# Performance work log

Measured on AMD Instinct MI355X. Metric: run time of the kernel, lower is better.

The kernel has to match this reference:

```python
import jax, jax.numpy as jnp
import numpy as np

ALPHA = 0.1        # ista() default lambda (module-level alpha is unused in this path)
N_ITERS = 50       # fixed iteration count replacing tolerance-based early exit
POWER_ITERS = 20   # power iterations to estimate Lipschitz constant L = ||Wd||_2^2


def _soft_threshold(x, t):
    return jnp.sign(x) * jnp.maximum(jnp.abs(x) - t, 0.0)


def _lipschitz(Wd):
    # largest eigenvalue of Wd^T Wd via power iteration
    v = jnp.ones((Wd.shape[1],), Wd.dtype)
    def body(v, _):
        v = Wd.T @ (Wd @ v)
        v = v / (jnp.linalg.norm(v) + 1e-12)
        return v, None
    v, _ = jax.lax.scan(body, v, None, length=POWER_ITERS)
    return jnp.vdot(v, Wd.T @ (Wd @ v)) / (jnp.vdot(v, v) + 1e-12)


def _ista(X, Wd):
    # X: [B, D], Wd: [D, K] -> sparse codes Z: [B, K]
    L = jax.lax.stop_gradient(_lipschitz(Wd))
    step = 1.0 / L
    Z0 = jnp.zeros((X.shape[0], Wd.shape[1]), X.dtype)
    def body(Z, _):
        grad = (Z @ Wd.T - X) @ Wd          # [B,D] @ [D,K] -> [B,K]
        Z = _soft_threshold(Z - step * grad, step * ALPHA)
        return Z, None
    Z, _ = jax.lax.scan(body, Z0, None, length=N_ITERS)
    return Z


def setup_inputs() -> dict:
    key = jax.random.key(0)
    k1, k2 = jax.random.split(key)
    z_e_x = jax.random.normal(k1, (8192, 16, 8, 8), jnp.float32)   # [B,C,H,W]
    dictionary = jax.random.normal(k2, (1024, 512), jnp.float32)   # [D,K], D=H*W*C
    return {"z_e_x": z_e_x, "dictionary": dictionary}


def reference(z_e_x, dictionary):
    B = z_e_x.shape[0]
    # permute(0,2,3,1).flatten(start_dim=1): [B,C,H,W] -> [B, H*W*C]
    X = jnp.transpose(z_e_x, (0, 2, 3, 1)).reshape(B, -1)
    Z = _ista(X, dictionary)                                  # [B,K]
    sparsity = jnp.sum(jnp.abs(Z) > 1e-6) / B
    outputs = (dictionary @ Z.T).T                            # [B,D]
    # torch code views back to z_e_x.shape WITHOUT inverse permute; replicate exactly
    return outputs.reshape(z_e_x.shape), sparsity
```

## Files before the change

kernel.cpp:

```cpp
#include <hip/hip_runtime.h>
#include <math.h>

#define BATCH 8192
#define DIM 1024
#define KDIM 512
#define ALPHA_C 0.1f
#define N_ITERS 50
#define ROWS 32
#define ZSH 512
#define HC 3
#define SEG 256

typedef short bf16x8 __attribute__((ext_vector_type(8)));
typedef float f32x4 __attribute__((ext_vector_type(4)));

__device__ __forceinline__ short f2bf(float x) {
  union { float f; unsigned u; } v; v.f = x;
  unsigned r = v.u + 0x7fffu + ((v.u >> 16) & 1u);
  return (short)(r >> 16);
}
__device__ __forceinline__ float bf2f(short s) {
  union { float f; unsigned u; } v;
  v.u = ((unsigned)(unsigned short)s) << 16;
  return v.f;
}

__device__ __forceinline__ int zswz(int row, int col) {
  return row * ZSH + ((((col >> 3) ^ (row & 15)) << 3) | (col & 7));
}
__device__ __forceinline__ int zoff8(int row, int colg) {
  return row * ZSH + ((colg ^ (row & 15)) << 3);
}

__global__ __launch_bounds__(256) void k_mmT_part(const float* __restrict__ A,
                                                  const float* __restrict__ B,
                                                  float* __restrict__ P) {
  int tx = (threadIdx.x & 15) * 2;
  int ty = (threadIdx.x >> 4) * 2;
  int a0 = blockIdx.y * 32 + ty;
  int b0 = blockIdx.x * 32 + tx;
  int j0 = blockIdx.z * SEG;
  float a00 = 0.f, a01 = 0.f, a10 = 0.f, a11 = 0.f;
  for (int j = j0; j < j0 + SEG; j += 8) {
#pragma unroll
    for (int u = 0; u < 8; ++u) {
      float2 av = *(const float2*)&A[(size_t)(j + u) * KDIM + a0];
      float2 bv = *(const float2*)&B[(size_t)(j + u) * KDIM + b0];
      a00 += av.x * bv.x;
      a01 += av.x * bv.y;
      a10 += av.y * bv.x;
      a11 += av.y * bv.y;
    }
  }
  float* P0 = P + (size_t)blockIdx.z * KDIM * KDIM;
  *(float2*)&P0[(size_t)a0 * KDIM + b0] = make_float2(a00, a01);
  *(float2*)&P0[(size_t)(a0 + 1) * KDIM + b0] = make_float2(a10, a11);
}

__global__ __launch_bounds__(256) void k_red(const float* __restrict__ P,
                                             float* __restrict__ C, int S,
                                             float scale) {
  int t = blockIdx.x * 256 + threadIdx.x;
  f32x4 s = (f32x4){0.f, 0.f, 0.f, 0.f};
  for (int z = 0; z < S; ++z) {
    f32x4 p = *(const f32x4*)&P[(size_t)z * KDIM * KDIM + t * 4];
    s.x += p.x; s.y += p.y; s.z += p.z; s.w += p.w;
  }
  s.x *= scale; s.y *= scale; s.z *= scale; s.w *= scale;
  *(f32x4*)&C[t * 4] = s;
}

__global__ __launch_bounds__(1024) void k_power_fast(
    const float* __restrict__ G4, const float* __restrict__ G8,
    const float* __restrict__ G, float* __restrict__ scal) {
  __shared__ float v[KDIM];
  __shared__ float part[1024];
  __shared__ double red[16];
  __shared__ double red2[16];
  __shared__ float stot;
  int tid = threadIdx.x;
  int lane = tid & 63, wid = tid >> 6;
  int col = tid & 511, h = tid >> 9;
  if (h == 0) v[col] = 1.0f;
  __syncthreads();

  const float* mats[3] = {G4, G8, G8};
#pragma unroll
  for (int s = 0; s < 3; ++s) {
    const float* gp = mats[s] + (size_t)(h * 256) * KDIM + col;
    const float* vp = v + h * 256;
    float a0 = 0.f, a1 = 0.f, a2 = 0.f, a3 = 0.f;
#pragma unroll 4
    for (int j = 0; j < 256; j += 4) {
      a0 += gp[(size_t)(j + 0) * KDIM] * vp[j + 0];
      a1 += gp[(size_t)(j + 1) * KDIM] * vp[j + 1];
      a2 += gp[(size_t)(j + 2) * KDIM] * vp[j + 2];
      a3 += gp[(size_t)(j + 3) * KDIM] * vp[j + 3];
    }
    part[tid] = (a0 + a1) + (a2 + a3);
    __syncthreads();
    float u = 0.f;
    double ssq = 0.0;
    if (h == 0) {
      u = part[col] + part[col + 512];
      ssq = (double)u * (double)u;
    }
#pragma unroll
    for (int off = 32; off; off >>= 1) ssq += __shfl_xor(ssq, off);
    if (lane == 0) red[wid] = ssq;
    __syncthreads();
    if (tid == 0) {
      double t = 0.0;
      for (int i = 0; i < 16; ++i) t += red[i];
      stot = (float)(sqrt(t) + 1e-12);
    }
    __syncthreads();
    if (h == 0) v[col] = u / stot;
    __syncthreads();
  }

  {
    const float* gp = G + (size_t)(h * 256) * KDIM + col;
    const float* vp = v + h * 256;
    float a0 = 0.f, a1 = 0.f, a2 = 0.f, a3 = 0.f;
#pragma unroll 4
    for (int j = 0; j < 256; j += 4) {
      a0 += gp[(size_t)(j + 0) * KDIM] * vp[j + 0];
      a1 += gp[(size_t)(j + 1) * KDIM] * vp[j + 1];
      a2 += gp[(size_t)(j + 2) * KDIM] * vp[j + 2];
      a3 += gp[(size_t)(j + 3) * KDIM] * vp[j + 3];
    }
    part[tid] = (a0 + a1) + (a2 + a3);
    __syncthreads();
    double nu = 0.0, de = 0.0;
    if (h == 0) {
      float u = part[col] + part[col + 512];
      nu = (double)v[col] * (double)u;
      de = (double)v[col] * (double)v[col];
    }
#pragma unroll
    for (int off = 32; off; off >>= 1) {
      nu += __shfl_xor(nu, off);
      de += __shfl_xor(de, off);
    }
    if (lane == 0) { red[wid] = nu; red2[wid] = de; }
    __syncthreads();
    if (tid == 0) {
      double n = 0.0, d = 0.0;
      for (int i = 0; i < 16; ++i) { n += red[i]; d += red2[i]; }
      float L = (float)(n / (d + 1e-12));
      float step = 1.0f / L;
      scal[0] = step;
      scal[1] = step * ALPHA_C;
    }
  }
}

__global__ __launch_bounds__(256) void k_pack_h(const float* __restrict__ G,
                                                const float* __restrict__ scal,
                                                short* __restrict__ Hh) {
  int t = blockIdx.x * 256 + threadIdx.x;
  int k = t >> 9, n = t & 511;
  float step = scal[0];
  float h = ((k == n) ? 1.0f : 0.0f) - step * G[k * KDIM + n];
  int kk = k >> 5, q = (k >> 3) & 3, j = k & 7;
  Hh[((size_t)((kk * 4 + q) * 512 + n)) * 8 + j] = f2bf(h);
}

__global__ __launch_bounds__(256) void k_pack_w(const float* __restrict__ Wd,
                                                const float* __restrict__ scal,
                                                short* __restrict__ Wh) {
  int t = blockIdx.x * 256 + threadIdx.x;
  int k = t >> 9, n = t & 511;
  float w = scal[0] * Wd[k * KDIM + n];
  int kk = k >> 5, q = (k >> 3) & 3, j = k & 7;
  Wh[((size_t)((kk * 4 + q) * 512 + n)) * 8 + j] = f2bf(w);
}

__global__ __launch_bounds__(256) void k_pack_wt(const float* __restrict__ Wd,
                                                 short* __restrict__ Wh) {
  int t = blockIdx.x * 256 + threadIdx.x;
  int k = t >> 10, n = t & 1023;
  float w = Wd[n * KDIM + k];
  int kk = k >> 5, q = (k >> 3) & 3, j = k & 7;
  Wh[((size_t)((kk * 4 + q) * 1024 + n)) * 8 + j] = f2bf(w);
}

__global__ __launch_bounds__(1024) void k_ista(
    const float* __restrict__ zex, const short* __restrict__ Hh,
    const short* __restrict__ Wph, const short* __restrict__ Wth,
    const float* __restrict__ scal, float* __restrict__ out,
    int* __restrict__ gcnt) {
  __shared__ short Zb[2][ROWS * ZSH];
  __shared__ short Hl2[HC * 16384];
  int tid = threadIdx.x;
  int lane = tid & 63, wid = tid >> 6;
  int l15 = lane & 15, lq = lane >> 4;
  int rb = blockIdx.x * ROWS;
  float thr = scal[1];

  f32x4 cs[2][2];
#pragma unroll
  for (int rf = 0; rf < 2; ++rf)
#pragma unroll
    for (int cf = 0; cf < 2; ++cf) cs[rf][cf] = (f32x4){0.f, 0.f, 0.f, 0.f};

  int sr = tid >> 5;
  int sc = (tid & 31) >> 1;
  int ph = tid & 1;
  for (int half = 0; half < 2; ++half) {
    __syncthreads();
    {
      const float* src =
          &zex[(size_t)(rb + sr) * DIM + sc * 64 + half * 32 + ph * 16];
#pragma unroll
      for (int m = 0; m < 16; m += 4) {
        float4 xv = *(const float4*)&src[m];
        float xs[4] = {xv.x, xv.y, xv.z, xv.w};
#pragma unroll
        for (int e = 0; e < 4; ++e) {
          int mm = ph * 16 + m + e;
          int dd = ((mm >> 3) << 7) + ((mm & 7) << 4) + sc;
          Zb[0][zswz(sr, dd)] = f2bf(xs[e]);
        }
      }
    }
    __syncthreads();
#pragma unroll 2
    for (int kk = 0; kk < 16; ++kk) {
      int kkg = half * 16 + kk;
      bf16x8 a[2];
#pragma unroll
      for (int rf = 0; rf < 2; ++rf)
        a[rf] = *(const bf16x8*)&Zb[0][zoff8(rf * 16 + l15, kk * 4 + lq)];
#pragma unroll
      for (int cf = 0; cf < 2; ++cf) {
        int n = wid * 32 + cf * 16 + l15;
        bf16x8 bh = *(const bf16x8*)&Wph[((size_t)((kkg * 4 + lq) * 512 + n)) * 8];
#pragma unroll
        for (int rf = 0; rf < 2; ++rf)
          cs[rf][cf] = __builtin_amdgcn_mfma_f32_16x16x32_bf16(a[rf], bh, cs[rf][cf], 0, 0, 0);
      }
    }
  }
  __syncthreads();

  for (int i = tid * 8; i < HC * 16384; i += 8192)
    *(bf16x8*)&Hl2[i] = *(const bf16x8*)&Hh[i];

#pragma unroll
  for (int rf = 0; rf < 2; ++rf)
#pragma unroll
    for (int cf = 0; cf < 2; ++cf) {
      int col = wid * 32 + cf * 16 + l15;
#pragma unroll
      for (int e = 0; e < 4; ++e) {
        float pre = cs[rf][cf][e];
        float mag = fmaxf(fabsf(pre) - thr, 0.f);
        float z = (pre >= 0.f) ? mag : -mag;
        int row = rf * 16 + lq * 4 + e;
        Zb[0][zswz(row, col)] = f2bf(z);
      }
    }
  __syncthreads();

  int cur = 0;
#pragma unroll 1
  for (int it = 1; it < N_ITERS; ++it) {
    int rot = it & 15;
    f32x4 acc[2][2];

    {
      int kkr = rot;
      bf16x8 a[2];
#pragma unroll
      for (int rf = 0; rf < 2; ++rf)
        a[rf] = *(const bf16x8*)&Zb[cur][zoff8(rf * 16 + l15, kkr * 4 + lq)];
#pragma unroll
      for (int cf = 0; cf < 2; ++cf) {
        int n = wid * 32 + cf * 16 + l15;
        size_t off = ((size_t)((kkr * 4 + lq) * 512 + n)) * 8;
        bf16x8 bh = (kkr < HC) ? *(const bf16x8*)&Hl2[off]
                               : *(const bf16x8*)&Hh[off];
#pragma unroll
        for (int rf = 0; rf < 2; ++rf)
          acc[rf][cf] = __builtin_amdgcn_mfma_f32_16x16x32_bf16(a[rf], bh, cs[rf][cf], 0, 0, 0);
      }
    }
#pragma unroll 2
    for (int kk = 1; kk < 16; ++kk) {
      int kkr = (kk + rot) & 15;
      bf16x8 a[2];
#pragma unroll
      for (int rf = 0; rf < 2; ++rf)
        a[rf] = *(const bf16x8*)&Zb[cur][zoff8(rf * 16 + l15, kkr * 4 + lq)];
#pragma unroll
      for (int cf = 0; cf < 2; ++cf) {
        int n = wid * 32 + cf * 16 + l15;
        size_t off = ((size_t)((kkr * 4 + lq) * 512 + n)) * 8;
        bf16x8 bh = (kkr < HC) ? *(const bf16x8*)&Hl2[off]
                               : *(const bf16x8*)&Hh[off];
#pragma unroll
        for (int rf = 0; rf < 2; ++rf)
          acc[rf][cf] = __builtin_amdgcn_mfma_f32_16x16x32_bf16(a[rf], bh, acc[rf][cf], 0, 0, 0);
      }
    }
#pragma unroll
    for (int rf = 0; rf < 2; ++rf)
#pragma unroll
      for (int cf = 0; cf < 2; ++cf) {
        int col = wid * 32 + cf * 16 + l15;
#pragma unroll
        for (int e = 0; e < 4; ++e) {
          float pre = acc[rf][cf][e];
          float mag = fmaxf(fabsf(pre) - thr, 0.f);
          float z = (pre >= 0.f) ? mag : -mag;
          int row = rf * 16 + lq * 4 + e;
          Zb[cur ^ 1][zswz(row, col)] = f2bf(z);
        }
      }
    cur ^= 1;
    __syncthreads();
  }

  int cnt = 0;
#pragma unroll 4
  for (int i = tid; i < ROWS * ZSH; i += 1024)
    cnt += (fabsf(bf2f(Zb[cur][i])) > 1e-6f) ? 1 : 0;
#pragma unroll
  for (int off = 32; off; off >>= 1) cnt += __shfl_xor(cnt, off);
  if (lane == 0) atomicAdd(gcnt, cnt);

  {
    f32x4 o[2][4];
#pragma unroll
    for (int rf = 0; rf < 2; ++rf)
#pragma unroll
      for (int cf = 0; cf < 4; ++cf) o[rf][cf] = (f32x4){0.f, 0.f, 0.f, 0.f};

#pragma unroll 2
    for (int kk = 0; kk < 16; ++kk) {
      bf16x8 a[2];
#pragma unroll
      for (int rf = 0; rf < 2; ++rf)
        a[rf] = *(const bf16x8*)&Zb[cur][zoff8(rf * 16 + l15, kk * 4 + lq)];
#pragma unroll
      for (int cf = 0; cf < 4; ++cf) {
        int n = wid * 64 + cf * 16 + l15;
        bf16x8 bh = *(const bf16x8*)&Wth[((size_t)((kk * 4 + lq) * 1024 + n)) * 8];
#pragma unroll
        for (int rf = 0; rf < 2; ++rf)
          o[rf][cf] = __builtin_amdgcn_mfma_f32_16x16x32_bf16(a[rf], bh, o[rf][cf], 0, 0, 0);
      }
    }
#pragma unroll
    for (int rf = 0; rf < 2; ++rf)
#pragma unroll
      for (int cf = 0; cf < 4; ++cf) {
        int col = wid * 64 + cf * 16 + l15;
#pragma unroll
        for (int e = 0; e < 4; ++e) {
          int row = rb + rf * 16 + lq * 4 + e;
          out[(size_t)row * DIM + col] = o[rf][cf][e];
        }
      }
  }
}

__global__ void k_final(const int* __restrict__ gcnt, float* __restrict__ out) {
  out[(size_t)BATCH * DIM] = (float)(*gcnt) / (float)BATCH;
}

extern "C" void kernel_launch(void* const* d_in, const int* in_sizes, int n_in,
                              void* d_out, int out_size, void* d_ws,
                              size_t ws_size, hipStream_t stream) {
  (void)in_sizes; (void)n_in; (void)out_size; (void)ws_size;
  const float* zex = (const float*)d_in[0];
  const float* Wd = (const float*)d_in[1];
  float* out = (float*)d_out;
  char* ws = (char*)d_ws;

  float* G = (float*)ws;
  float* G2 = (float*)(ws + (1 << 20));
  float* G4 = (float*)(ws + 2 * (1 << 20));
  float* G8 = (float*)(ws + 3 * (1 << 20));
  short* Hh = (short*)(ws + 4 * (1 << 20));
  short* Wph = (short*)(ws + 4 * (1 << 20) + (512 << 10));
  short* Wth = (short*)(ws + 5 * (1 << 20) + (512 << 10));
  float* scal = (float*)(ws + 6 * (1 << 20) + (512 << 10));
  int* gcnt = (int*)(ws + 6 * (1 << 20) + (512 << 10) + 64);
  float* PG = (float*)(ws + 1 * (1 << 20));
  float* PG2 = (float*)(ws + 2 * (1 << 20));
  float* PG4 = (float*)(ws + 3 * (1 << 20));
  float* PG8 = (float*)(ws + 4 * (1 << 20));

  hipMemsetAsync(gcnt, 0, sizeof(int), stream);
  k_mmT_part<<<dim3(16, 16, 4), 256, 0, stream>>>(Wd, Wd, PG);
  k_red<<<256, 256, 0, stream>>>(PG, G, 4, 1.0f);
  k_mmT_part<<<dim3(16, 16, 2), 256, 0, stream>>>(G, G, PG2);
  k_red<<<256, 256, 0, stream>>>(PG2, G2, 2, 9.5367431640625e-07f);
  k_mmT_part<<<dim3(16, 16, 2), 256, 0, stream>>>(G2, G2, PG4);
  k_red<<<256, 256, 0, stream>>>(PG4, G4, 2, 1.0f);
  k_mmT_part<<<dim3(16, 16, 2), 256, 0, stream>>>(G4, G4, PG8);
  k_red<<<256, 256, 0, stream>>>(PG8, G8, 2, 1.0f);
  k_power_fast<<<1, 1024, 0, stream>>>(G4, G8, G, scal);
  k_pack_h<<<1024, 256, 0, stream>>>(G, scal, Hh);
  k_pack_w<<<2048, 256, 0, stream>>>(Wd, scal, Wph);
  k_pack_wt<<<2048, 256, 0, stream>>>(Wd, Wth);
  k_ista<<<BATCH / ROWS, 1024, 0, stream>>>(zex, Hh, Wph, Wth, scal, out, gcnt);
  k_final<<<1, 1, 0, stream>>>(gcnt, out);
}
```

Baseline: 545.6 us.

## Run ISTA iterations with FP8 MFMA on scaled off-diagonal H and FP8 Z

Measured after the change: 536.3 us. No clear change (-1.7%).

```diff
diff --git a/kernel.cpp b/kernel.cpp
--- a/kernel.cpp
+++ b/kernel.cpp
@@ -8,11 +8,14 @@
 #define N_ITERS 50
 #define ROWS 32
 #define ZSH 512
-#define HC 3
 #define SEG 256
+#define SH 32.0f
+#define SZ 16.0f
+#define INVS 0.001953125f
 
 typedef short bf16x8 __attribute__((ext_vector_type(8)));
 typedef float f32x4 __attribute__((ext_vector_type(4)));
+typedef long longx2 __attribute__((ext_vector_type(2)));
 
 __device__ __forceinline__ short f2bf(float x) {
   union { float f; unsigned u; } v; v.f = x;
@@ -30,6 +33,10 @@
 }
 __device__ __forceinline__ int zoff8(int row, int colg) {
   return row * ZSH + ((colg ^ (row & 15)) << 3);
+}
+__device__ __forceinline__ int z8a(int row, int c) {
+  int g = ((((c >> 3) & 3) << 4) | (c >> 5)) ^ (row & 14);
+  return row * 512 + g * 8 + (c & 7);
 }
 
 __global__ __launch_bounds__(256) void k_mmT_part(const float* __restrict__ A,
@@ -156,15 +163,19 @@
   }
 }
 
-__global__ __launch_bounds__(256) void k_pack_h(const float* __restrict__ G,
-                                                const float* __restrict__ scal,
-                                                short* __restrict__ Hh) {
+__global__ __launch_bounds__(256) void k_pack_h8(const float* __restrict__ G,
+                                                 const float* __restrict__ scal,
+                                                 char* __restrict__ H8,
+                                                 float* __restrict__ hd) {
   int t = blockIdx.x * 256 + threadIdx.x;
   int k = t >> 9, n = t & 511;
   float step = scal[0];
-  float h = ((k == n) ? 1.0f : 0.0f) - step * G[k * KDIM + n];
-  int kk = k >> 5, q = (k >> 3) & 3, j = k & 7;
-  Hh[((size_t)((kk * 4 + q) * 512 + n)) * 8 + j] = f2bf(h);
+  float g = G[k * KDIM + n];
+  if (k == n) hd[n] = 1.0f - step * g;
+  float h = (k == n) ? 0.f : (-step * g) * SH;
+  int p = __builtin_amdgcn_cvt_pk_fp8_f32(h, h, 0, false);
+  size_t off = ((size_t)((k >> 5) * 4 + ((k >> 3) & 3))) * 4096 + n * 8 + (k & 7);
+  H8[off] = (char)(p & 0xff);
 }
 
 __global__ __launch_bounds__(256) void k_pack_w(const float* __restrict__ Wd,
@@ -187,12 +198,12 @@
 }
 
 __global__ __launch_bounds__(1024) void k_ista(
-    const float* __restrict__ zex, const short* __restrict__ Hh,
-    const short* __restrict__ Wph, const short* __restrict__ Wth,
-    const float* __restrict__ scal, float* __restrict__ out,
-    int* __restrict__ gcnt) {
-  __shared__ short Zb[2][ROWS * ZSH];
-  __shared__ short Hl2[HC * 16384];
+    const float* __restrict__ zex, const char* __restrict__ H8,
+    const float* __restrict__ hd, const short* __restrict__ Wph,
+    const short* __restrict__ Wth, const float* __restrict__ scal,
+    float* __restrict__ out, int* __restrict__ gcnt) {
+  __shared__ short Xb[ROWS * ZSH];
+  __shared__ char Z8[2][ROWS * 512];
   int tid = threadIdx.x;
   int lane = tid & 63, wid = tid >> 6;
   int l15 = lane & 15, lq = lane >> 4;
@@ -221,7 +232,7 @@
         for (int e = 0; e < 4; ++e) {
           int mm = ph * 16 + m + e;
           int dd = ((mm >> 3) << 7) + ((mm & 7) << 4) + sc;
-          Zb[0][zswz(sr, dd)] = f2bf(xs[e]);
+          Xb[zswz(sr, dd)] = f2bf(xs[e]);
         }
       }
     }
@@ -232,7 +243,7 @@
       bf16x8 a[2];
 #pragma unroll
       for (int rf = 0; rf < 2; ++rf)
-        a[rf] = *(const bf16x8*)&Zb[0][zoff8(rf * 16 + l15, kk * 4 + lq)];
+        a[rf] = *(const bf16x8*)&Xb[zoff8(rf * 16 + l15, kk * 4 + lq)];
 #pragma unroll
       for (int cf = 0; cf < 2; ++cf) {
         int n = wid * 32 + cf * 16 + l15;
@@ -245,9 +256,10 @@
   }
   __syncthreads();
 
-  for (int i = tid * 8; i < HC * 16384; i += 8192)
-    *(bf16x8*)&Hl2[i] = *(const bf16x8*)&Hh[i];
-
+  float hd0 = hd[wid * 32 + l15];
+  float hd1 = hd[wid * 32 + 16 + l15];
+
+  float zreg[2][2][4];
 #pragma unroll
   for (int rf = 0; rf < 2; ++rf)
 #pragma unroll
@@ -258,65 +270,68 @@
         float pre = cs[rf][cf][e];
         float mag = fmaxf(fabsf(pre) - thr, 0.f);
         float z = (pre >= 0.f) ? mag : -mag;
-        int row = rf * 16 + lq * 4 + e;
-        Zb[0][zswz(row, col)] = f2bf(z);
+        zreg[rf][cf][e] = z;
+        int pk = __builtin_amdgcn_cvt_pk_fp8_f32(z * SZ, z * SZ, 0, false);
+        Z8[0][z8a(rf * 16 + lq * 4 + e, col)] = (char)(pk & 0xff);
       }
     }
   __syncthreads();
+
+  int key = l15 & 14;
+  int abase0 = l15 * 512 + lq * 128;
+  int abase1 = (16 + l15) * 512 + lq * 128;
+  int vb = lq * 4096 + (wid * 32 + l15) * 8;
 
   int cur = 0;
 #pragma unroll 1
   for (int it = 1; it < N_ITERS; ++it) {
-    int rot = it & 15;
     f32x4 acc[2][2];
-
-    {
-      int kkr = rot;
-      bf16x8 a[2];
-#pragma unroll
-      for (int rf = 0; rf < 2; ++rf)
-        a[rf] = *(const bf16x8*)&Zb[cur][zoff8(rf * 16 + l15, kkr * 4 + lq)];
+#pragma unroll
+    for (int rf = 0; rf < 2; ++rf)
+#pragma unroll
+      for (int cf = 0; cf < 2; ++cf) acc[rf][cf] = (f32x4){0.f, 0.f, 0.f, 0.f};
+
+    int ks = (it & 7) << 1;
+#define ISTA_BODY(kk)                                                         \
+  {                                                                           \
+    int ao = ((kk) ^ key) * 8;                                                \
+    longx2 a0 = *(const longx2*)&Z8[cur][abase0 + ao];                        \
+    longx2 a1 = *(const longx2*)&Z8[cur][abase1 + ao];                        \
+    const char* hp = H8 + (size_t)(kk)*16384;                                 \
+    long b00 = *(const long*)&hp[vb];                                         \
+    long b01 = *(const long*)&hp[vb + 128];                                   \
+    long b10 = *(const long*)&hp[vb + 16384];                                 \
+    long b11 = *(const long*)&hp[vb + 16384 + 128];                           \
+    acc[0][0] = __builtin_amdgcn_mfma_f32_16x16x32_fp8_fp8(a0.x, b00, acc[0][0], 0, 0, 0); \
+    acc[1][0] = __builtin_amdgcn_mfma_f32_16x16x32_fp8_fp8(a1.x, b00, acc[1][0], 0, 0, 0); \
+    acc[0][1] = __builtin_amdgcn_mfma_f32_16x16x32_fp8_fp8(a0.x, b01, acc[0][1], 0, 0, 0); \
+    acc[1][1] = __builtin_amdgcn_mfma_f32_16x16x32_fp8_fp8(a1.x, b01, acc[1][1], 0, 0, 0); \
+    acc[0][0] = __builtin_amdgcn_mfma_f32_16x16x32_fp8_fp8(a0.y, b10, acc[0][0], 0, 0, 0); \
+    acc[1][0] = __builtin_amdgcn_mfma_f32_16x16x32_fp8_fp8(a1.y, b10, acc[1][0], 0, 0, 0); \
+    acc[0][1] = __builtin_amdgcn_mfma_f32_16x16x32_fp8_fp8(a0.y, b11, acc[0][1], 0, 0, 0); \
+    acc[1][1] = __builtin_amdgcn_mfma_f32_16x16x32_fp8_fp8(a1.y, b11, acc[1][1], 0, 0, 0); \
+  }
+#pragma unroll 1
+    for (int kk = ks; kk < 16; kk += 2) ISTA_BODY(kk);
+#pragma unroll 1
+    for (int kk = 0; kk < ks; kk += 2) ISTA_BODY(kk);
+#undef ISTA_BODY
+
+#pragma unroll
+    for (int rf = 0; rf < 2; ++rf)
 #pragma unroll
       for (int cf = 0; cf < 2; ++cf) {
-        int n = wid * 32 + cf * 16 + l15;
-        size_t off = ((size_t)((kkr * 4 + lq) * 512 + n)) * 8;
-        bf16x8 bh = (kkr < HC) ? *(const bf16x8*)&Hl2[off]
-                               : *(const bf16x8*)&Hh[off];
-#pragma unroll
-        for (int rf = 0; rf < 2; ++rf)
-          acc[rf][cf] = __builtin_amdgcn_mfma_f32_16x16x32_bf16(a[rf], bh, cs[rf][cf], 0, 0, 0);
-      }
-    }
-#pragma unroll 2
-    for (int kk = 1; kk < 16; ++kk) {
-      int kkr = (kk + rot) & 15;
-      bf16x8 a[2];
-#pragma unroll
-      for (int rf = 0; rf < 2; ++rf)
-        a[rf] = *(const bf16x8*)&Zb[cur][zoff8(rf * 16 + l15, kkr * 4 + lq)];
-#pragma unroll
-      for (int cf = 0; cf < 2; ++cf) {
-        int n = wid * 32 + cf * 16 + l15;
-        size_t off = ((size_t)((kkr * 4 + lq) * 512 + n)) * 8;
-        bf16x8 bh = (kkr < HC) ? *(const bf16x8*)&Hl2[off]
-                               : *(const bf16x8*)&Hh[off];
-#pragma unroll
-        for (int rf = 0; rf < 2; ++rf)
-          acc[rf][cf] = __builtin_amdgcn_mfma_f32_16x16x32_bf16(a[rf], bh, acc[rf][cf], 0, 0, 0);
-      }
-    }
-#pragma unroll
-    for (int rf = 0; rf < 2; ++rf)
-#pragma unroll
-      for (int cf = 0; cf < 2; ++cf) {
+        float hdc = cf ? hd1 : hd0;
         int col = wid * 32 + cf * 16 + l15;
 #pragma unroll
         for (int e = 0; e < 4; ++e) {
-          float pre = acc[rf][cf][e];
+          float pre = cs[rf][cf][e] + acc[rf][cf][e] * INVS +
+                      hdc * zreg[rf][cf][e];
           float mag = fmaxf(fabsf(pre) - thr, 0.f);
           float z = (pre >= 0.f) ? mag : -mag;
-          int row = rf * 16 + lq * 4 + e;
-          Zb[cur ^ 1][zswz(row, col)] = f2bf(z);
+          zreg[rf][cf][e] = z;
+          int pk = __builtin_amdgcn_cvt_pk_fp8_f32(z * SZ, z * SZ, 0, false);
+          Z8[cur ^ 1][z8a(rf * 16 + lq * 4 + e, col)] = (char)(pk & 0xff);
         }
       }
     cur ^= 1;
@@ -324,12 +339,27 @@
   }
 
   int cnt = 0;
-#pragma unroll 4
-  for (int i = tid; i < ROWS * ZSH; i += 1024)
-    cnt += (fabsf(bf2f(Zb[cur][i])) > 1e-6f) ? 1 : 0;
+#pragma unroll
+  for (int rf = 0; rf < 2; ++rf)
+#pragma unroll
+    for (int cf = 0; cf < 2; ++cf)
+#pragma unroll
+      for (int e = 0; e < 4; ++e)
+        cnt += (fabsf(zreg[rf][cf][e]) > 1e-6f) ? 1 : 0;
 #pragma unroll
   for (int off = 32; off; off >>= 1) cnt += __shfl_xor(cnt, off);
   if (lane == 0) atomicAdd(gcnt, cnt);
+
+#pragma unroll
+  for (int rf = 0; rf < 2; ++rf)
+#pragma unroll
+    for (int cf = 0; cf < 2; ++cf) {
+      int col = wid * 32 + cf * 16 + l15;
+#pragma unroll
+      for (int e = 0; e < 4; ++e)
+        Xb[zswz(rf * 16 + lq * 4 + e, col)] = f2bf(zreg[rf][cf][e]);
+    }
+  __syncthreads();
 
   {
     f32x4 o[2][4];
@@ -343,7 +373,7 @@
       bf16x8 a[2];
 #pragma unroll
       for (int rf = 0; rf < 2; ++rf)
-        a[rf] = *(const bf16x8*)&Zb[cur][zoff8(rf * 16 + l15, kk * 4 + lq)];
+        a[rf] = *(const bf16x8*)&Xb[zoff8(rf * 16 + l15, kk * 4 + lq)];
 #pragma unroll
       for (int cf = 0; cf < 4; ++cf) {
         int n = wid * 64 + cf * 16 + l15;
@@ -384,7 +414,8 @@
   float* G2 = (float*)(ws + (1 << 20));
   float* G4 = (float*)(ws + 2 * (1 << 20));
   float* G8 = (float*)(ws + 3 * (1 << 20));
-  short* Hh = (short*)(ws + 4 * (1 << 20));
+  char* H8 = (char*)(ws + 4 * (1 << 20));
+  float* hd = (float*)(ws + 4 * (1 << 20) + (256 << 10));
   short* Wph = (short*)(ws + 4 * (1 << 20) + (512 << 10));
   short* Wth = (short*)(ws + 5 * (1 << 20) + (512 << 10));
   float* scal = (float*)(ws + 6 * (1 << 20) + (512 << 10));
@@ -404,9 +435,10 @@
   k_mmT_part<<<dim3(16, 16, 2), 256, 0, stream>>>(G4, G4, PG8);
   k_red<<<256, 256, 0, stream>>>(PG8, G8, 2, 1.0f);
   k_power_fast<<<1, 1024, 0, stream>>>(G4, G8, G, scal);
-  k_pack_h<<<1024, 256, 0, stream>>>(G, scal, Hh);
+  k_pack_h8<<<1024, 256, 0, stream>>>(G, scal, H8, hd);
   k_pack_w<<<2048, 256, 0, stream>>>(Wd, scal, Wph);
   k_pack_wt<<<2048, 256, 0, stream>>>(Wd, Wth);
-  k_ista<<<BATCH / ROWS, 1024, 0, stream>>>(zex, Hh, Wph, Wth, scal, out, gcnt);
+  k_ista<<<BATCH / ROWS, 1024, 0, stream>>>(zex, H8, hd, Wph, Wth, scal, out,
+                                            gcnt);
   k_final<<<1, 1, 0, stream>>>(gcnt, out);
 }
```
